# Performance work log

Hardware: AMD Instinct MI355X
Metric: run time of the kernel (lower is better)

The kernel has to match this reference:

```python
import jax, jax.numpy as jnp
import numpy as np

B, N, D = 16, 512, 256
HEADS = 8
HIDEF = 1024
BLOCK, WINDOW = 32, 64
LEVELS = 5
PYOUT = 128
NCLS, NANCH = 5, 9
NEG = -1e9


def _sinusoidal_pos(n, d):
    # PositionEmbeddingStatic: deterministic sinusoidal table [n, d]
    pos = np.arange(n)[:, None].astype(np.float64)
    i = np.arange(d)[None, :]
    angle = pos / np.power(10000.0, (2 * (i // 2)) / d)
    pe = np.where(i % 2 == 0, np.sin(angle), np.cos(angle))
    return jnp.asarray(pe, jnp.float32)


def _layernorm(x, g, b, eps=1e-5):
    m = x.mean(-1, keepdims=True)
    v = x.var(-1, keepdims=True)
    return (x - m) * jax.lax.rsqrt(v + eps) * g + b


def _bn(x_bcn, g, b, eps=1e-5):
    # BatchNorm1d in training mode: per-channel batch stats over (B, N)
    m = x_bcn.mean((0, 2), keepdims=True)
    v = x_bcn.var((0, 2), keepdims=True)
    return (x_bcn - m) * jax.lax.rsqrt(v + eps) * g[None, :, None] + b[None, :, None]


def _sparse_attention(x, Wqkv, bqkv, Wo, bo):
    # Windowed block-sparse attention: queries in block i attend to key blocks
    # [i-w, i+w] with w = window_size // block_size. Never materializes SxS.
    Bx, Nx, Dx = x.shape
    H, dh = HEADS, Dx // HEADS
    nb, bs = Nx // BLOCK, BLOCK
    w = WINDOW // BLOCK
    qkv = x @ Wqkv + bqkv
    q, k, v = jnp.split(qkv, 3, axis=-1)

    def to_blocks(t):  # [B,N,D] -> [B,H,nb,bs,dh]
        return t.reshape(Bx, nb, bs, H, dh).transpose(0, 3, 1, 2, 4)

    q, k, v = to_blocks(q), to_blocks(k), to_blocks(v)
    offs = list(range(-w, w + 1))
    # roll by -o puts key block (i+o) at query-block position i
    k_band = jnp.concatenate([jnp.roll(k, -o, axis=2) for o in offs], axis=3)
    v_band = jnp.concatenate([jnp.roll(v, -o, axis=2) for o in offs], axis=3)
    blk = jnp.arange(nb)
    valid = jnp.concatenate(
        [jnp.repeat(((blk + o >= 0) & (blk + o < nb))[:, None], bs, axis=1) for o in offs],
        axis=1)  # [nb, (2w+1)*bs]
    scale = 1.0 / jnp.sqrt(jnp.asarray(dh, x.dtype))
    scores = jnp.einsum('bhnqd,bhnkd->bhnqk', q, k_band) * scale
    scores = jnp.where(valid[None, None, :, None, :], scores, NEG)
    p = jax.nn.softmax(scores, axis=-1)
    o = jnp.einsum('bhnqk,bhnkd->bhnqd', p, v_band)
    o = o.transpose(0, 2, 3, 1, 4).reshape(Bx, Nx, Dx)
    return o @ Wo + bo


def setup_inputs():
    key = jax.random.key(0)
    ks = iter(jax.random.split(key, 48))
    g = lambda shape, s=0.02: jax.random.normal(next(ks), shape, jnp.float32) * s
    z = lambda *shape: jnp.zeros(shape, jnp.float32)
    o = lambda *shape: jnp.ones(shape, jnp.float32)
    return {
        'x': jax.random.normal(next(ks), (B, N, D), jnp.float32),
        'patch_W': g((D, D)), 'patch_b': z(D),
        'ln_g': o(D), 'ln_b': z(D),
        'ff_W1': g((D, HIDEF)), 'ff_b1': z(HIDEF),
        'ff_W2': g((HIDEF, D)), 'ff_b2': z(D),
        'Wqkv': g((D, 3 * D)), 'bqkv': z(3 * D),
        'Wo': g((D, D)), 'bo': z(D),
        'bn1_g': o(D), 'bn1_b': z(D),
        'bn2_g': o(D), 'bn2_b': z(D),
        'pyr_W': g((LEVELS, D, PYOUT)), 'pyr_b': z(LEVELS, PYOUT),
        'fcl_W': g((LEVELS * PYOUT * N, 128), 0.005), 'fcl_b': z(128),
        'addbn_g': o(128), 'addbn_b': z(128),
        'cls_W1': g((128, 256)), 'cls_b1': z(256),
        'cls_W2': g((256, NCLS * NANCH)), 'cls_b2': z(NCLS * NANCH),
        'box_W1': g((128, 128)), 'box_b1': z(128),
        'box_W2': g((128, 4 * NANCH)), 'box_b2': z(4 * NANCH),
    }


def reference(x, patch_W, patch_b, ln_g, ln_b, ff_W1, ff_b1, ff_W2, ff_b2,
              Wqkv, bqkv, Wo, bo, bn1_g, bn1_b, bn2_g, bn2_b,
              pyr_W, pyr_b, fcl_W, fcl_b, addbn_g, addbn_b,
              cls_W1, cls_b1, cls_W2, cls_b2, box_W1, box_b1, box_W2, box_b2):
    pos = _sinusoidal_pos(N, D)

    def ff(h):
        return jax.nn.gelu(h @ ff_W1 + ff_b1) @ ff_W2 + ff_b2

    def mnt(h):
        h = _layernorm(h @ patch_W + patch_b, ln_g, ln_b)  # patch embed + norm
        h = h + pos[None]
        idt = h
        h = ff(h)
        h = _sparse_attention(h, Wqkv, bqkv, Wo, bo)
        h = h + idt
        h = _bn(h.transpose(0, 2, 1), bn1_g, bn1_b).transpose(0, 2, 1)
        idt = h
        h = ff(h) + idt
        h = _bn(h.transpose(0, 2, 1), bn2_g, bn2_b).transpose(0, 2, 1)
        return h

    outs = []
    for _ in range(5):
        x = mnt(x)
        outs.append(x.transpose(0, 2, 1))  # [B, D, N]

    # pyramid: per-level 1x1 conv D -> 128
    feats = [jnp.einsum('bdn,dc->bcn', outs[i], pyr_W[i]) + pyr_b[i][None, :, None]
             for i in range(LEVELS)]
    flat = jnp.concatenate([f.reshape(f.shape[0], -1) for f in feats], axis=1)
    add = (flat @ fcl_W + fcl_b)[:, :, None]          # [B,128,1]
    add = _bn(add, addbn_g, addbn_b).transpose(0, 2, 1)  # [B,1,128]
    cls = jax.nn.relu(add @ cls_W1 + cls_b1) @ cls_W2 + cls_b2
    cls = jax.nn.softmax(cls, axis=-1).reshape(-1, NANCH, NCLS)  # eval mode softmax
    box = (jax.nn.relu(add @ box_W1 + box_b1) @ box_W2 + box_b2).reshape(-1, NANCH, 4)
    return jnp.concatenate([cls, box], axis=-1)  # [B, NANCH, NCLS+4]
```

## Files before the change

### kernel.cpp

```cpp
#include <hip/hip_runtime.h>
#include <hip/hip_bf16.h>
#include <math.h>

#define B_ 16
#define N_ 512
#define D_ 256
#define HEADS_ 8
#define DH_ 32
#define HIDEF_ 1024
#define NBLK_ 16
#define BS_ 32
#define LEVELS_ 5
#define PYOUT_ 128
#define ROWS_ (B_ * N_)
#define FCL_K 327680
#define FCL_KB 256
#define FCL_CHUNKS 1280

typedef __attribute__((ext_vector_type(8))) short short8;
typedef __attribute__((ext_vector_type(4))) short short4v;
typedef __attribute__((ext_vector_type(4))) unsigned short ushort4v;
typedef __attribute__((ext_vector_type(4))) float f32x4;

__device__ __forceinline__ float bf2f(short u) {
    return __uint_as_float(((unsigned int)(unsigned short)u) << 16);
}
__device__ __forceinline__ unsigned short f2bf(float x) {
    __hip_bfloat16 h = __float2bfloat16(x);
    return *reinterpret_cast<unsigned short*>(&h);
}

__device__ __forceinline__ float gelu_f(float x) {
    float x3 = x * x * x;
    return 0.5f * x * (1.f + tanhf(0.7978845608028654f * (x + 0.044715f * x3)));
}

__global__ __launch_bounds__(256) void prep_kernel(
    const float* __restrict__ patch_W, const float* __restrict__ Wqkv,
    const float* __restrict__ Wo, const float* __restrict__ ff_W1,
    const float* __restrict__ ff_W2, const float* __restrict__ pyr_W,
    const float* __restrict__ x_in,
    __hip_bfloat16* __restrict__ patchWt, __hip_bfloat16* __restrict__ qkvWt,
    __hip_bfloat16* __restrict__ WoWt, __hip_bfloat16* __restrict__ W1t,
    __hip_bfloat16* __restrict__ W2t, __hip_bfloat16* __restrict__ pyrWt,
    float* __restrict__ pos, __hip_bfloat16* __restrict__ Xb) {
    __shared__ float tt[32][33];
    int bid = blockIdx.x, t = threadIdx.x;
    if (bid >= 1504) {
        int base = (bid - 1504) * 2048 + t * 8;
        float4 a = *(const float4*)&x_in[base];
        float4 b = *(const float4*)&x_in[base + 4];
        ushort4v u0 = {f2bf(a.x), f2bf(a.y), f2bf(a.z), f2bf(a.w)};
        ushort4v u1 = {f2bf(b.x), f2bf(b.y), f2bf(b.z), f2bf(b.w)};
        *(ushort4v*)((short*)Xb + base) = u0;
        *(ushort4v*)((short*)Xb + base + 4) = u1;
        return;
    }
    if (bid >= 992) {
        int idx = (bid - 992) * 256 + t;
        int n = idx >> 8, i = idx & 255;
        double angle = (double)n / pow(10000.0, (double)(2 * (i >> 1)) / 256.0);
        pos[idx] = (float)((i & 1) ? cos(angle) : sin(angle));
        return;
    }
    const float* W; __hip_bfloat16* Wt; int K, N, bx, by;
    if (bid < 64)       { W = patch_W; Wt = patchWt; K = 256; N = 256; bx = bid % 8; by = bid / 8; }
    else if (bid < 256) { int l = bid - 64;  W = Wqkv;  Wt = qkvWt; K = 256; N = 768;  bx = l % 24; by = l / 24; }
    else if (bid < 320) { int l = bid - 256; W = Wo;    Wt = WoWt;  K = 256; N = 256;  bx = l % 8;  by = l / 8; }
    else if (bid < 576) { int l = bid - 320; W = ff_W1; Wt = W1t;   K = 256; N = 1024; bx = l % 32; by = l / 32; }
    else if (bid < 832) { int l = bid - 576; W = ff_W2; Wt = W2t;   K = 1024; N = 256; bx = l % 8;  by = l / 8; }
    else                { int l = bid - 832; int z = l / 32; int r = l % 32;
                          W = pyr_W + (size_t)z * 256 * 128; Wt = pyrWt + (size_t)z * 256 * 128;
                          K = 256; N = 128; bx = r % 4; by = r / 4; }
    int bx32 = bx * 32, by32 = by * 32;
    int tx = t & 31, ty = t >> 5;
#pragma unroll
    for (int i = 0; i < 32; i += 8)
        tt[ty + i][tx] = W[(size_t)(by32 + ty + i) * N + bx32 + tx];
    __syncthreads();
#pragma unroll
    for (int i = 0; i < 32; i += 8)
        Wt[(size_t)(bx32 + ty + i) * K + by32 + tx] = __float2bfloat16(tt[tx][ty + i]);
}

template <int ACT, bool OUTF, bool OUTB, bool STATS, int BM, int BN>
__global__ __launch_bounds__(256) void bgemm_kernel(
    const __hip_bfloat16* __restrict__ A, const __hip_bfloat16* __restrict__ Wt,
    const float* __restrict__ bias, const float* __restrict__ resid,
    float* __restrict__ C, __hip_bfloat16* __restrict__ Cb, int M, int Nn, int K,
    float* __restrict__ bnp) {
    __shared__ __hip_bfloat16 Alds[2][BM * 64];
    __shared__ __hip_bfloat16 Blds[2][BN * 64];
    constexpr int WM_ = (BM == 128 && BN == 64) ? 4 : 2;
    constexpr int WN_ = 4 / WM_;
    constexpr int WH = BM / WM_;
    constexpr int WC = BN / WN_;
    constexpr int MW = WH / 16;
    constexpr int NW = WC / 16;
    constexpr int AR = BM / 32;
    constexpr int BR = BN / 32;
    int tid = threadIdx.x;
    int wid = tid >> 6, lane = tid & 63;
    int flat = blockIdx.y * gridDim.x + blockIdx.x;
    int q8 = (gridDim.x * gridDim.y) >> 3;
    int wg = (flat & 7) * q8 + (flat >> 3);
    int bx = wg % gridDim.x, by = wg / gridDim.x;
    int row0 = by * BM, col0 = bx * BN;
    int wr = wid / WN_, wc = wid % WN_;
    int r16 = lane & 15, kq = lane >> 4;

    f32x4 acc[MW][NW];
#pragma unroll
    for (int m = 0; m < MW; m++)
#pragma unroll
        for (int n = 0; n < NW; n++) acc[m][n] = (f32x4){0.f, 0.f, 0.f, 0.f};

    auto stage = [&](int b, int k0) {
#pragma unroll
        for (int i = 0; i < AR; i++) {
            int slot = i * 256 + tid;
            int row = slot >> 3, qp = slot & 7;
            int q = qp ^ ((row >> 1) & 7);
            const __hip_bfloat16* ga = A + (size_t)(row0 + row) * K + k0 + q * 8;
            __builtin_amdgcn_global_load_lds(
                (const __attribute__((address_space(1))) void*)ga,
                (__attribute__((address_space(3))) void*)((char*)&Alds[b][0] + i * 4096 + wid * 1024),
                16, 0, 0);
        }
#pragma unroll
        for (int i = 0; i < BR; i++) {
            int slot = i * 256 + tid;
            int row = slot >> 3, qp = slot & 7;
            int q = qp ^ ((row >> 1) & 7);
            const __hip_bfloat16* gb = Wt + (size_t)(col0 + row) * K + k0 + q * 8;
            __builtin_amdgcn_global_load_lds(
                (const __attribute__((address_space(1))) void*)gb,
                (__attribute__((address_space(3))) void*)((char*)&Blds[b][0] + i * 4096 + wid * 1024),
                16, 0, 0);
        }
    };

    stage(0, 0);
    __syncthreads();
    int cur = 0;
    for (int k0 = 0; k0 < K; k0 += 64) {
        if (k0 + 64 < K) stage(cur ^ 1, k0 + 64);
#pragma unroll
        for (int h = 0; h < 2; h++) {
            short8 af[MW], bf4[NW];
#pragma unroll
            for (int m = 0; m < MW; m++) {
                int row = wr * WH + m * 16 + r16;
                int phys = (h * 4 + kq) ^ ((row >> 1) & 7);
                af[m] = *reinterpret_cast<const short8*>(
                    reinterpret_cast<const char*>(&Alds[cur][0]) + row * 128 + phys * 16);
            }
#pragma unroll
            for (int n = 0; n < NW; n++) {
                int row = wc * WC + n * 16 + r16;
                int phys = (h * 4 + kq) ^ ((row >> 1) & 7);
                bf4[n] = *reinterpret_cast<const short8*>(
                    reinterpret_cast<const char*>(&Blds[cur][0]) + row * 128 + phys * 16);
            }
#pragma unroll
            for (int m = 0; m < MW; m++)
#pragma unroll
                for (int n = 0; n < NW; n++)
                    acc[m][n] = __builtin_amdgcn_mfma_f32_16x16x32_bf16(af[m], bf4[n], acc[m][n], 0, 0, 0);
        }
        __syncthreads();
        cur ^= 1;
    }

    int rg = lane >> 4;
    float s1a[NW], s2a[NW];
#pragma unroll
    for (int n = 0; n < NW; n++) { s1a[n] = 0.f; s2a[n] = 0.f; }
#pragma unroll
    for (int n = 0; n < NW; n++) {
        int cc = col0 + wc * WC + n * 16 + r16;
        float bv = bias[cc];
#pragma unroll
        for (int m = 0; m < MW; m++) {
            int rb = row0 + wr * WH + m * 16 + rg * 4;
#pragma unroll
            for (int j = 0; j < 4; j++) {
                int r = rb + j;
                float v = acc[m][n][j] + bv;
                if (resid) v += resid[(size_t)r * Nn + cc];
                if (ACT == 1) v = gelu_f(v);
                if (OUTF) C[(size_t)r * Nn + cc] = v;
                if (OUTB) Cb[(size_t)r * Nn + cc] = __float2bfloat16(v);
                if (STATS) { s1a[n] += v; s2a[n] += v * v; }
            }
        }
    }
    if (STATS) {
        float* sc = (float*)&Alds[0][0];
        int part = wid * 4 + rg;
#pragma unroll
        for (int n = 0; n < NW; n++) {
            int c = wc * WC + n * 16 + r16;
            sc[c * 16 + part] = s1a[n];
            sc[BN * 16 + c * 16 + part] = s2a[n];
        }
        __syncthreads();
        if (tid < BN) {
            float a = 0.f, b2 = 0.f;
#pragma unroll
            for (int p = 0; p < 16; p++) {
                a += sc[tid * 16 + p];
                b2 += sc[BN * 16 + tid * 16 + p];
            }
            bnp[by * 256 + col0 + tid] = a;
            bnp[32768 + by * 256 + col0 + tid] = b2;
        }
    }
}

__global__ __launch_bounds__(256) void patchln_kernel(
    const __hip_bfloat16* __restrict__ A, const __hip_bfloat16* __restrict__ Wt,
    const float* __restrict__ bias, const float* __restrict__ lng,
    const float* __restrict__ lnb, const float* __restrict__ pos,
    float* __restrict__ H, __hip_bfloat16* __restrict__ Hb) {
    __shared__ char __attribute__((aligned(16))) smem[73728];
    float (*Cls)[260] = (float(*)[260])smem;
    int tid = threadIdx.x;
    int wid = tid >> 6, lane = tid & 63;
    int row0 = blockIdx.x * 32;
    int r16 = lane & 15, kq = lane >> 4, g = lane >> 4;

    f32x4 acc[2][4];
#pragma unroll
    for (int m = 0; m < 2; m++)
#pragma unroll
        for (int n = 0; n < 4; n++) acc[m][n] = (f32x4){0.f, 0.f, 0.f, 0.f};

    auto stage = [&](int b, int k0) {
        {
            int row = tid >> 3, qp = tid & 7;
            int q = qp ^ ((row >> 1) & 7);
            const __hip_bfloat16* ga = A + (size_t)(row0 + row) * 256 + k0 + q * 8;
            __builtin_amdgcn_global_load_lds(
                (const __attribute__((address_space(1))) void*)ga,
                (__attribute__((address_space(3))) void*)(smem + b * 4096 + wid * 1024),
                16, 0, 0);
        }
#pragma unroll
        for (int i = 0; i < 8; i++) {
            int slot = i * 256 + tid;
            int row = slot >> 3, qp = slot & 7;
            int q = qp ^ ((row >> 1) & 7);
            const __hip_bfloat16* gb = Wt + (size_t)row * 256 + k0 + q * 8;
            __builtin_amdgcn_global_load_lds(
                (const __attribute__((address_space(1))) void*)gb,
                (__attribute__((address_space(3))) void*)(smem + 8192 + b * 32768 + i * 4096 + wid * 1024),
                16, 0, 0);
        }
    };

    stage(0, 0);
    __syncthreads();
    int cur = 0;
    for (int k0 = 0; k0 < 256; k0 += 64) {
        if (k0 + 64 < 256) stage(cur ^ 1, k0 + 64);
        const char* Ab = smem + cur * 4096;
        const char* Bb = smem + 8192 + cur * 32768;
#pragma unroll
        for (int h = 0; h < 2; h++) {
            short8 af[2], bf4[4];
#pragma unroll
            for (int m = 0; m < 2; m++) {
                int row = m * 16 + r16;
                int phys = (h * 4 + kq) ^ ((row >> 1) & 7);
                af[m] = *reinterpret_cast<const short8*>(Ab + row * 128 + phys * 16);
            }
#pragma unroll
            for (int n = 0; n < 4; n++) {
                int row = wid * 64 + n * 16 + r16;
                int phys = (h * 4 + kq) ^ ((row >> 1) & 7);
                bf4[n] = *reinterpret_cast<const short8*>(Bb + row * 128 + phys * 16);
            }
#pragma unroll
            for (int m = 0; m < 2; m++)
#pragma unroll
                for (int n = 0; n < 4; n++)
                    acc[m][n] = __builtin_amdgcn_mfma_f32_16x16x32_bf16(af[m], bf4[n], acc[m][n], 0, 0, 0);
        }
        __syncthreads();
        cur ^= 1;
    }
#pragma unroll
    for (int n = 0; n < 4; n++) {
        int col = wid * 64 + n * 16 + r16;
        float bv = bias[col];
#pragma unroll
        for (int m = 0; m < 2; m++)
#pragma unroll
            for (int j = 0; j < 4; j++)
                Cls[m * 16 + g * 4 + j][col] = acc[m][n][j] + bv;
    }
    __syncthreads();
    float4 g4 = ((const float4*)lng)[lane];
    float4 b4 = ((const float4*)lnb)[lane];
#pragma unroll
    for (int rr = 0; rr < 8; rr++) {
        int r = wid * 8 + rr;
        float4 v = *(const float4*)&Cls[r][lane * 4];
        float s = v.x + v.y + v.z + v.w;
#pragma unroll
        for (int mk = 32; mk; mk >>= 1) s += __shfl_xor(s, mk);
        float mean = s * (1.f / 256.f);
        float dx = v.x - mean, dy = v.y - mean, dz = v.z - mean, dw = v.w - mean;
        float q = dx * dx + dy * dy + dz * dz + dw * dw;
#pragma unroll
        for (int mk = 32; mk; mk >>= 1) q += __shfl_xor(q, mk);
        float rstd = rsqrtf(q * (1.f / 256.f) + 1e-5f);
        int grow = row0 + r;
        float4 p4 = ((const float4*)pos)[(size_t)(grow & (N_ - 1)) * 64 + lane];
        float o0 = dx * rstd * g4.x + b4.x + p4.x;
        float o1 = dy * rstd * g4.y + b4.y + p4.y;
        float o2 = dz * rstd * g4.z + b4.z + p4.z;
        float o3 = dw * rstd * g4.w + b4.w + p4.w;
        ((float4*)(H + (size_t)grow * D_))[lane] = (float4){o0, o1, o2, o3};
        ushort4v u = {f2bf(o0), f2bf(o1), f2bf(o2), f2bf(o3)};
        *((ushort4v*)(Hb + (size_t)grow * D_) + lane) = u;
    }
}

template <bool DO_PATCH>
__global__ __launch_bounds__(256) void bnpatch_kernel(
    const float* __restrict__ T, const float* __restrict__ bnp,
    const float* __restrict__ bng, const float* __restrict__ bnb,
    const __hip_bfloat16* __restrict__ patchWt, const float* __restrict__ patch_b,
    const float* __restrict__ lng, const float* __restrict__ lnb,
    const float* __restrict__ pos,
    const __hip_bfloat16* __restrict__ pyrWt_l, const float* __restrict__ pyr_b_l,
    int level, float* __restrict__ FLAT,
    float* __restrict__ H, __hip_bfloat16* __restrict__ Hb) {
    __shared__ char __attribute__((aligned(16))) smem[68096];
    float* sm = (float*)(smem + 66048);
    float* sv = sm + 256;
    int tid = threadIdx.x;
    int wid = tid >> 6, lane = tid & 63;
    int row0 = blockIdx.x * 32;
    int r16 = lane & 15, kq = lane >> 4, g = lane >> 4;
    int wr = wid >> 1, wc = wid & 1;

    {
        float s = 0.f, s2 = 0.f;
#pragma unroll 4
        for (int yy = 0; yy < 128; yy++) {
            s += bnp[yy * 256 + tid];
            s2 += bnp[32768 + yy * 256 + tid];
        }
        float m = s * (1.f / 8192.f);
        sm[tid] = m;
        sv[tid] = rsqrtf(s2 * (1.f / 8192.f) - m * m + 1e-5f);
    }
    __syncthreads();
    {
        float4 m4 = ((const float4*)sm)[lane];
        float4 r4 = ((const float4*)sv)[lane];
        float4 g4 = ((const float4*)bng)[lane];
        float4 b4 = ((const float4*)bnb)[lane];
#pragma unroll
        for (int rr = 0; rr < 8; rr++) {
            int r = wid * 8 + rr;
            float4 x4 = ((const float4*)(T + (size_t)(row0 + r) * D_))[lane];
            float o0 = (x4.x - m4.x) * r4.x * g4.x + b4.x;
            float o1 = (x4.y - m4.y) * r4.y * g4.y + b4.y;
            float o2 = (x4.z - m4.z) * r4.z * g4.z + b4.z;
            float o3 = (x4.w - m4.w) * r4.w * g4.w + b4.w;
            ushort4v u = {f2bf(o0), f2bf(o1), f2bf(o2), f2bf(o3)};
            int c = lane >> 1;
            int phys = c ^ (r & 7);
            *(ushort4v*)(smem + r * 512 + phys * 16 + (lane & 1) * 8) = u;
        }
    }
    __syncthreads();

    if (DO_PATCH) {
        f32x4 acc[8];
#pragma unroll
        for (int n = 0; n < 8; n++) acc[n] = (f32x4){0.f, 0.f, 0.f, 0.f};
        for (int k0 = 0; k0 < 256; k0 += 64) {
#pragma unroll
            for (int i = 0; i < 8; i++) {
                int slot = i * 256 + tid;
                int row = slot >> 3, qp = slot & 7;
                int q = qp ^ ((row >> 1) & 7);
                const __hip_bfloat16* gb = patchWt + (size_t)row * 256 + k0 + q * 8;
                __builtin_amdgcn_global_load_lds(
                    (const __attribute__((address_space(1))) void*)gb,
                    (__attribute__((address_space(3))) void*)(smem + 16384 + i * 4096 + wid * 1024),
                    16, 0, 0);
            }
            __syncthreads();
#pragma unroll
            for (int h = 0; h < 2; h++) {
                int arow = wr * 16 + r16;
                int ac = (k0 >> 3) + h * 4 + kq;
                int aphys = ac ^ (arow & 7);
                short8 af = *(const short8*)(smem + arow * 512 + aphys * 16);
                short8 bf4[8];
#pragma unroll
                for (int n = 0; n < 8; n++) {
                    int brow = wc * 128 + n * 16 + r16;
                    int bphys = (h * 4 + kq) ^ ((brow >> 1) & 7);
                    bf4[n] = *(const short8*)(smem + 16384 + brow * 128 + bphys * 16);
                }
#pragma unroll
                for (int n = 0; n < 8; n++)
                    acc[n] = __builtin_amdgcn_mfma_f32_16x16x32_bf16(af, bf4[n], acc[n], 0, 0, 0);
            }
            __syncthreads();
        }
        float (*Cls)[260] = (float(*)[260])(smem + 16384);
#pragma unroll
        for (int n = 0; n < 8; n++) {
            int col = wc * 128 + n * 16 + r16;
            float bv = patch_b[col];
#pragma unroll
            for (int j = 0; j < 4; j++)
                Cls[wr * 16 + g * 4 + j][col] = acc[n][j] + bv;
        }
        __syncthreads();
        float4 g4 = ((const float4*)lng)[lane];
        float4 b4 = ((const float4*)lnb)[lane];
#pragma unroll
        for (int rr = 0; rr < 8; rr++) {
            int r = wid * 8 + rr;
            float4 v = *(const float4*)&Cls[r][lane * 4];
            float s = v.x + v.y + v.z + v.w;
#pragma unroll
            for (int mk = 32; mk; mk >>= 1) s += __shfl_xor(s, mk);
            float mean = s * (1.f / 256.f);
            float dx = v.x - mean, dy = v.y - mean, dz = v.z - mean, dw = v.w - mean;
            float q = dx * dx + dy * dy + dz * dz + dw * dw;
#pragma unroll
            for (int mk = 32; mk; mk >>= 1) q += __shfl_xor(q, mk);
            float rstd = rsqrtf(q * (1.f / 256.f) + 1e-5f);
            int grow = row0 + r;
            float4 p4 = ((const float4*)pos)[(size_t)(grow & (N_ - 1)) * 64 + lane];
            float o0 = dx * rstd * g4.x + b4.x + p4.x;
            float o1 = dy * rstd * g4.y + b4.y + p4.y;
            float o2 = dz * rstd * g4.z + b4.z + p4.z;
            float o3 = dw * rstd * g4.w + b4.w + p4.w;
            ((float4*)(H + (size_t)grow * D_))[lane] = (float4){o0, o1, o2, o3};
            ushort4v u = {f2bf(o0), f2bf(o1), f2bf(o2), f2bf(o3)};
            *((ushort4v*)(Hb + (size_t)grow * D_) + lane) = u;
        }
    }

    f32x4 pacc[4];
#pragma unroll
    for (int n = 0; n < 4; n++) pacc[n] = (f32x4){0.f, 0.f, 0.f, 0.f};
    for (int k0 = 0; k0 < 256; k0 += 64) {
#pragma unroll
        for (int i = 0; i < 4; i++) {
            int slot = i * 256 + tid;
            int row = slot >> 3, qp = slot & 7;
            int q = qp ^ ((row >> 1) & 7);
            const __hip_bfloat16* gb = pyrWt_l + (size_t)row * 256 + k0 + q * 8;
            __builtin_amdgcn_global_load_lds(
                (const __attribute__((address_space(1))) void*)gb,
                (__attribute__((address_space(3))) void*)(smem + 49664 + i * 4096 + wid * 1024),
                16, 0, 0);
        }
        __syncthreads();
#pragma unroll
        for (int h = 0; h < 2; h++) {
            int arow = wr * 16 + r16;
            int ac = (k0 >> 3) + h * 4 + kq;
            int aphys = ac ^ (arow & 7);
            short8 af = *(const short8*)(smem + arow * 512 + aphys * 16);
            short8 bf4[4];
#pragma unroll
            for (int n = 0; n < 4; n++) {
                int brow = wc * 64 + n * 16 + r16;
                int bphys = (h * 4 + kq) ^ ((brow >> 1) & 7);
                bf4[n] = *(const short8*)(smem + 49664 + brow * 128 + bphys * 16);
            }
#pragma unroll
            for (int n = 0; n < 4; n++)
                pacc[n] = __builtin_amdgcn_mfma_f32_16x16x32_bf16(af, bf4[n], pacc[n], 0, 0, 0);
        }
        __syncthreads();
    }
    float (*olds)[33] = (float(*)[33])(smem + 16384);
#pragma unroll
    for (int n = 0; n < 4; n++) {
        int ch = wc * 64 + n * 16 + r16;
        float bv = pyr_b_l[ch];
#pragma unroll
        for (int j = 0; j < 4; j++)
            olds[ch][wr * 16 + g * 4 + j] = pacc[n][j] + bv;
    }
    __syncthreads();
    {
        int ch = tid >> 1, half = tid & 1;
        int bb = row0 >> 9, nn0 = (row0 & 511) + half * 16;
        float* dst = FLAT + (size_t)bb * 327680 + (size_t)(level * 128 + ch) * 512 + nn0;
        const float* src = &olds[ch][half * 16];
#pragma unroll
        for (int q = 0; q < 4; q++)
            *(float4*)(dst + q * 4) = *(const float4*)(src + q * 4);
    }
}

__global__ __launch_bounds__(256) void bn_applyfin_kernel(
    const float* __restrict__ x, const float* __restrict__ bnp, int prows,
    const float* __restrict__ g, const float* __restrict__ b,
    float* __restrict__ y, __hip_bfloat16* __restrict__ yb) {
    int tid = threadIdx.x;
    __shared__ float sm[256], sv[256];
    {
        float s = 0.f, s2 = 0.f;
#pragma unroll 4
        for (int yy = 0; yy < prows; yy++) {
            s += bnp[yy * 256 + tid];
            s2 += bnp[32768 + yy * 256 + tid];
        }
        float m = s * (1.f / 8192.f);
        sm[tid] = m;
        sv[tid] = rsqrtf(s2 * (1.f / 8192.f) - m * m + 1e-5f);
    }
    __syncthreads();
    int lane = tid & 63, w = tid >> 6;
    int row0 = blockIdx.x * 32;
    float4 m4 = *(const float4*)&sm[lane * 4];
    float4 r4 = *(const float4*)&sv[lane * 4];
    float4 g4 = ((const float4*)g)[lane];
    float4 b4 = ((const float4*)b)[lane];
#pragma unroll
    for (int rr = 0; rr < 8; rr++) {
        int row = row0 + w * 8 + rr;
        float4 x4 = ((const float4*)(x + (size_t)row * D_))[lane];
        float o0 = (x4.x - m4.x) * r4.x * g4.x + b4.x;
        float o1 = (x4.y - m4.y) * r4.y * g4.y + b4.y;
        float o2 = (x4.z - m4.z) * r4.z * g4.z + b4.z;
        float o3 = (x4.w - m4.w) * r4.w * g4.w + b4.w;
        if (y) ((float4*)(y + (size_t)row * D_))[lane] = (float4){o0, o1, o2, o3};
        if (yb) {
            ushort4v u = {f2bf(o0), f2bf(o1), f2bf(o2), f2bf(o3)};
            *((ushort4v*)(yb + (size_t)row * D_) + lane) = u;
        }
    }
}

__global__ __launch_bounds__(256) void attn_kernel(
    const __hip_bfloat16* __restrict__ qkv, __hip_bfloat16* __restrict__ outb) {
    int bx = blockIdx.x, h = blockIdx.y, b = blockIdx.z;
    int tid = threadIdx.x;
    int wid = tid >> 6, lane = tid & 63;
    __shared__ __hip_bfloat16 Klds[256 * 32];
    __shared__ __hip_bfloat16 Vt[32 * 264];
    const short* q16 = (const short*)qkv;

#pragma unroll
    for (int r = 0; r < 4; r++) {
        int slot = r * 256 + tid;
        int row = slot >> 2, qp = slot & 3;
        int ql = qp ^ ((row >> 1) & 3);
        int jb = bx * 4 - 2 + (row >> 5);
        jb = jb < 0 ? 0 : (jb > 15 ? 15 : jb);
        const short* ga = q16 + ((size_t)(b * N_ + jb * 32 + (row & 31))) * 768 + 256 + h * 32 + ql * 8;
        __builtin_amdgcn_global_load_lds(
            (const __attribute__((address_space(1))) void*)ga,
            (__attribute__((address_space(3))) void*)((char*)Klds + r * 4096 + wid * 1024),
            16, 0, 0);
    }
    {
        int row = tid;
        int jb = bx * 4 - 2 + (row >> 5);
        jb = jb < 0 ? 0 : (jb > 15 ? 15 : jb);
        const short* gv = q16 + ((size_t)(b * N_ + jb * 32 + (row & 31))) * 768 + 512 + h * 32;
        short8 v0 = *(const short8*)(gv);
        short8 v1 = *(const short8*)(gv + 8);
        short8 v2 = *(const short8*)(gv + 16);
        short8 v3 = *(const short8*)(gv + 24);
        short* vt = (short*)Vt;
#pragma unroll
        for (int e = 0; e < 8; e++) {
            vt[(e) * 264 + row] = v0[e];
            vt[(8 + e) * 264 + row] = v1[e];
            vt[(16 + e) * 264 + row] = v2[e];
            vt[(24 + e) * 264 + row] = v3[e];
        }
    }
    __syncthreads();

    int i = bx * 4 + wid;
    int c = lane & 15, g = lane >> 4;
    const float scale = 0.17677669529663687f;

#pragma unroll
    for (int qt = 0; qt < 2; qt++) {
        const short* qa = q16 + ((size_t)(b * N_ + i * 32 + qt * 16 + c)) * 768 + h * 32 + g * 8;
        short8 bq = *(const short8*)qa;
        f32x4 st[10];
#pragma unroll
        for (int t = 0; t < 10; t++) {
            int jb = i - 2 + (t >> 1);
            if (jb >= 0 && jb < NBLK_) {
                int row = wid * 32 + t * 16 + c;
                int phys = g ^ ((row >> 1) & 3);
                short8 ak = *(const short8*)((const char*)Klds + row * 64 + phys * 16);
                st[t] = __builtin_amdgcn_mfma_f32_16x16x32_bf16(
                    ak, bq, (f32x4){0.f, 0.f, 0.f, 0.f}, 0, 0, 0);
            }
        }
        float mx = -1e30f;
#pragma unroll
        for (int t = 0; t < 10; t++) {
            int jb = i - 2 + (t >> 1);
            if (jb >= 0 && jb < NBLK_) {
#pragma unroll
                for (int j = 0; j < 4; j++) {
                    st[t][j] *= scale;
                    mx = fmaxf(mx, st[t][j]);
                }
            }
        }
        mx = fmaxf(mx, __shfl_xor(mx, 16));
        mx = fmaxf(mx, __shfl_xor(mx, 32));
        float sum = 0.f;
#pragma unroll
        for (int t = 0; t < 10; t++) {
            int jb = i - 2 + (t >> 1);
            if (jb >= 0 && jb < NBLK_) {
#pragma unroll
                for (int j = 0; j < 4; j++) {
                    float e = __expf(st[t][j] - mx);
                    st[t][j] = e;
                    sum += e;
                }
            }
        }
        sum += __shfl_xor(sum, 16);
        sum += __shfl_xor(sum, 32);
        float inv = 1.f / sum;
        f32x4 o0 = (f32x4){0.f, 0.f, 0.f, 0.f};
        f32x4 o1 = (f32x4){0.f, 0.f, 0.f, 0.f};
        const short* vt = (const short*)Vt;
#pragma unroll
        for (int t = 0; t < 10; t++) {
            int jb = i - 2 + (t >> 1);
            if (jb >= 0 && jb < NBLK_) {
                short8 pa = (short8)0;
#pragma unroll
                for (int j = 0; j < 4; j++) pa[j] = (short)f2bf(st[t][j] * inv);
                int kb = wid * 32 + t * 16 + g * 4;
                short4v vb0 = *(const short4v*)(vt + (0 * 16 + c) * 264 + kb);
                short4v vb1 = *(const short4v*)(vt + (1 * 16 + c) * 264 + kb);
                short8 b0 = (short8)0, b1 = (short8)0;
#pragma unroll
                for (int e = 0; e < 4; e++) { b0[e] = vb0[e]; b1[e] = vb1[e]; }
                o0 = __builtin_amdgcn_mfma_f32_16x16x32_bf16(pa, b0, o0, 0, 0, 0);
                o1 = __builtin_amdgcn_mfma_f32_16x16x32_bf16(pa, b1, o1, 0, 0, 0);
            }
        }
#pragma unroll
        for (int j = 0; j < 4; j++) {
            size_t rbase = ((size_t)(b * N_ + i * 32 + qt * 16 + g * 4 + j)) * D_ + h * DH_;
            outb[rbase + c] = __float2bfloat16(o0[j]);
            outb[rbase + 16 + c] = __float2bfloat16(o1[j]);
        }
    }
}

__global__ __launch_bounds__(256) void fcl_partial_kernel(
    const float* __restrict__ flat, const float* __restrict__ W,
    float* __restrict__ partial) {
    int chunk = blockIdx.x;
    int t = threadIdx.x;
    int k0 = chunk * FCL_KB;
    __shared__ float fl[FCL_KB][20];
#pragma unroll
    for (int b = 0; b < 16; b++)
        fl[t][b] = flat[(size_t)b * FCL_K + k0 + t];
    __syncthreads();
    int j = t & 127, bg = t >> 7;
    f32x4 a0 = (f32x4){0.f, 0.f, 0.f, 0.f};
    f32x4 a1 = (f32x4){0.f, 0.f, 0.f, 0.f};
#pragma unroll 8
    for (int k = 0; k < FCL_KB; k++) {
        float w = W[(size_t)(k0 + k) * 128 + j];
        f32x4 f0 = *(const f32x4*)&fl[k][bg * 8];
        f32x4 f1 = *(const f32x4*)&fl[k][bg * 8 + 4];
        a0 += f0 * w;
        a1 += f1 * w;
    }
#pragma unroll
    for (int bi = 0; bi < 4; bi++) {
        partial[((size_t)chunk * 16 + bg * 8 + bi) * 128 + j] = a0[bi];
        partial[((size_t)chunk * 16 + bg * 8 + 4 + bi) * 128 + j] = a1[bi];
    }
}

__global__ __launch_bounds__(256) void fcl_reduce_kernel(
    const float* __restrict__ partial, const float* __restrict__ fcl_b,
    float* __restrict__ add) {
    int c0 = blockIdx.x * 32;
    int t = threadIdx.x;
    int ry = t >> 5, cx = t & 31;
    float s = 0.f;
    for (int r = ry; r < FCL_CHUNKS; r += 8)
        s += partial[(size_t)r * 2048 + c0 + cx];
    __shared__ float red[8][32];
    red[ry][cx] = s; __syncthreads();
    if (ry == 0) {
        float tot = 0.f;
#pragma unroll
        for (int q = 0; q < 8; q++) tot += red[q][cx];
        int col = c0 + cx;
        add[col] = tot + fcl_b[col & 127];
    }
}

__global__ __launch_bounds__(256) void head_kernel(
    const float* __restrict__ add, const float* __restrict__ abg, const float* __restrict__ abb,
    const float* __restrict__ cls_W1, const float* __restrict__ cls_b1,
    const float* __restrict__ cls_W2, const float* __restrict__ cls_b2,
    const float* __restrict__ box_W1, const float* __restrict__ box_b1,
    const float* __restrict__ box_W2, const float* __restrict__ box_b2,
    float* __restrict__ out) {
    __shared__ float a2[16][128];
    __shared__ float cm[16][256];
    __shared__ float cls[16][45];
    __shared__ float bmid[16][128];
    __shared__ float smden[16];
    int t = threadIdx.x;
    if (t < 128) {
        float m = 0.f;
#pragma unroll
        for (int b = 0; b < 16; b++) m += add[b * 128 + t];
        m *= (1.f / 16.f);
        float v = 0.f;
#pragma unroll
        for (int b = 0; b < 16; b++) { float d = add[b * 128 + t] - m; v += d * d; }
        v *= (1.f / 16.f);
        float sc = rsqrtf(v + 1e-5f) * abg[t];
#pragma unroll
        for (int b = 0; b < 16; b++) a2[b][t] = (add[b * 128 + t] - m) * sc + abb[t];
    }
    __syncthreads();
    for (int idx = t; idx < 4096; idx += 256) {
        int m = idx >> 8, c = idx & 255;
        float a = cls_b1[c];
        for (int k = 0; k < 128; k++) a += a2[m][k] * cls_W1[k * 256 + c];
        cm[m][c] = fmaxf(a, 0.f);
    }
    for (int idx = t; idx < 2048; idx += 256) {
        int m = idx >> 7, c = idx & 127;
        float a = box_b1[c];
        for (int k = 0; k < 128; k++) a += a2[m][k] * box_W1[k * 128 + c];
        bmid[m][c] = fmaxf(a, 0.f);
    }
    __syncthreads();
    for (int idx = t; idx < 720; idx += 256) {
        int m = idx / 45, c = idx % 45;
        float a = cls_b2[c];
        for (int k = 0; k < 256; k++) a += cm[m][k] * cls_W2[k * 45 + c];
        cls[m][c] = a;
    }
    __syncthreads();
    if (t < 16) {
        float mx = -1e30f;
        for (int c = 0; c < 45; c++) mx = fmaxf(mx, cls[t][c]);
        float s = 0.f;
        for (int c = 0; c < 45; c++) { float e = expf(cls[t][c] - mx); cls[t][c] = e; s += e; }
        smden[t] = s;
    }
    for (int idx = t; idx < 576; idx += 256) {
        int m = idx / 36, c = idx % 36;
        float a = box_b2[c];
        for (int k = 0; k < 128; k++) a += bmid[m][k] * box_W2[k * 36 + c];
        out[m * 81 + (c >> 2) * 9 + 5 + (c & 3)] = a;
    }
    __syncthreads();
    for (int idx = t; idx < 720; idx += 256) {
        int m = idx / 45, c = idx % 45;
        out[m * 81 + (c / 5) * 9 + (c % 5)] = cls[m][c] / smden[m];
    }
}

extern "C" void kernel_launch(void* const* d_in, const int* in_sizes, int n_in,
                              void* d_out, int out_size, void* d_ws, size_t ws_size,
                              hipStream_t stream) {
    const float* x_in    = (const float*)d_in[0];
    const float* patch_W = (const float*)d_in[1];
    const float* patch_b = (const float*)d_in[2];
    const float* ln_g    = (const float*)d_in[3];
    const float* ln_b    = (const float*)d_in[4];
    const float* ff_W1   = (const float*)d_in[5];
    const float* ff_b1   = (const float*)d_in[6];
    const float* ff_W2   = (const float*)d_in[7];
    const float* ff_b2   = (const float*)d_in[8];
    const float* Wqkv    = (const float*)d_in[9];
    const float* bqkv    = (const float*)d_in[10];
    const float* Wo      = (const float*)d_in[11];
    const float* bo      = (const float*)d_in[12];
    const float* bn1_g   = (const float*)d_in[13];
    const float* bn1_b   = (const float*)d_in[14];
    const float* bn2_g   = (const float*)d_in[15];
    const float* bn2_b   = (const float*)d_in[16];
    const float* pyr_W   = (const float*)d_in[17];
    const float* pyr_b   = (const float*)d_in[18];
    const float* fcl_W   = (const float*)d_in[19];
    const float* fcl_b   = (const float*)d_in[20];
    const float* addbn_g = (const float*)d_in[21];
    const float* addbn_b = (const float*)d_in[22];
    const float* cls_W1  = (const float*)d_in[23];
    const float* cls_b1  = (const float*)d_in[24];
    const float* cls_W2  = (const float*)d_in[25];
    const float* cls_b2  = (const float*)d_in[26];
    const float* box_W1  = (const float*)d_in[27];
    const float* box_b1  = (const float*)d_in[28];
    const float* box_W2  = (const float*)d_in[29];
    const float* box_b2  = (const float*)d_in[30];
    float* out = (float*)d_out;

    float* ws = (float*)d_ws;
    size_t off = 0;
    float* POS   = ws + off; off += 131072;
    float* H     = ws + off; off += 2097152;
    float* T     = ws + off; off += 2097152;
    float* UNION = ws + off; off += 4194304;
    float* FLAT  = ws + off; off += 5242880;
    float* PART  = ws + off; off += (size_t)FCL_CHUNKS * 2048;
    float* BNP   = ws + off; off += 2 * 32768;
    float* ADD   = ws + off; off += 2048;
    __hip_bfloat16* Hb   = (__hip_bfloat16*)(ws + off); off += 1048576;
    __hip_bfloat16* Tb   = (__hip_bfloat16*)(ws + off); off += 1048576;
    __hip_bfloat16* Xb   = (__hip_bfloat16*)(ws + off); off += 1048576;
    __hip_bfloat16* ATb  = (__hip_bfloat16*)(ws + off); off += 1048576;
    __hip_bfloat16* patchWt = (__hip_bfloat16*)(ws + off); off += 32768;
    __hip_bfloat16* qkvWt   = (__hip_bfloat16*)(ws + off); off += 98304;
    __hip_bfloat16* WoWt    = (__hip_bfloat16*)(ws + off); off += 32768;
    __hip_bfloat16* W1t     = (__hip_bfloat16*)(ws + off); off += 131072;
    __hip_bfloat16* W2t     = (__hip_bfloat16*)(ws + off); off += 131072;
    __hip_bfloat16* pyrWt   = (__hip_bfloat16*)(ws + off); off += 81920;
    __hip_bfloat16* MIDb = (__hip_bfloat16*)UNION;
    __hip_bfloat16* QKVb = (__hip_bfloat16*)UNION;

    prep_kernel<<<2528, 256, 0, stream>>>(
        patch_W, Wqkv, Wo, ff_W1, ff_W2, pyr_W, x_in,
        patchWt, qkvWt, WoWt, W1t, W2t, pyrWt, POS, Xb);

    patchln_kernel<<<256, 256, 0, stream>>>(Xb, patchWt, patch_b, ln_g, ln_b, POS, H, Hb);

    for (int it = 0; it < 5; it++) {
        bgemm_kernel<1, false, true, false, 128, 128><<<dim3(8, 64), 256, 0, stream>>>(
            Hb, W1t, ff_b1, nullptr, nullptr, MIDb, ROWS_, HIDEF_, D_, nullptr);
        bgemm_kernel<0, false, true, false, 64, 64><<<dim3(4, 128), 256, 0, stream>>>(
            MIDb, W2t, ff_b2, nullptr, nullptr, Tb, ROWS_, D_, HIDEF_, nullptr);
        bgemm_kernel<0, false, true, false, 128, 64><<<dim3(12, 64), 256, 0, stream>>>(
            Tb, qkvWt, bqkv, nullptr, nullptr, QKVb, ROWS_, 768, D_, nullptr);
        attn_kernel<<<dim3(4, HEADS_, B_), 256, 0, stream>>>(QKVb, ATb);
        bgemm_kernel<0, true, false, true, 64, 64><<<dim3(4, 128), 256, 0, stream>>>(
            ATb, WoWt, bo, H, T, nullptr, ROWS_, D_, D_, BNP);
        bn_applyfin_kernel<<<256, 256, 0, stream>>>(T, BNP, 128, bn1_g, bn1_b, H, Hb);
        bgemm_kernel<1, false, true, false, 128, 128><<<dim3(8, 64), 256, 0, stream>>>(
            Hb, W1t, ff_b1, nullptr, nullptr, MIDb, ROWS_, HIDEF_, D_, nullptr);
        bgemm_kernel<0, true, false, true, 64, 64><<<dim3(4, 128), 256, 0, stream>>>(
            MIDb, W2t, ff_b2, H, T, nullptr, ROWS_, D_, HIDEF_, BNP);
        if (it < 4) {
            bnpatch_kernel<true><<<256, 256, 0, stream>>>(
                T, BNP, bn2_g, bn2_b, patchWt, patch_b, ln_g, ln_b, POS,
                pyrWt + (size_t)it * D_ * PYOUT_, pyr_b + it * PYOUT_, it, FLAT, H, Hb);
        } else {
            bnpatch_kernel<false><<<256, 256, 0, stream>>>(
                T, BNP, bn2_g, bn2_b, patchWt, patch_b, ln_g, ln_b, POS,
                pyrWt + (size_t)it * D_ * PYOUT_, pyr_b + it * PYOUT_, it, FLAT, H, Hb);
        }
    }

    fcl_partial_kernel<<<FCL_CHUNKS, 256, 0, stream>>>(FLAT, fcl_W, PART);
    fcl_reduce_kernel<<<64, 256, 0, stream>>>(PART, fcl_b, ADD);
    head_kernel<<<1, 256, 0, stream>>>(ADD, addbn_g, addbn_b,
        cls_W1, cls_b1, cls_W2, cls_b2, box_W1, box_b1, box_W2, box_b2, out);
    (void)in_sizes; (void)n_in; (void)out_size; (void)ws_size;
}
```

Before: 873.1 us.

## Fuse BatchNorm apply into first FFN GEMM prologue

Replaces the separate BN1 apply kernel and the following FFN up-projection GEMM with one kernel. Each 64x128 tile recomputes the BN statistics from the partial sums, normalizes its 64 rows of T into swizzled LDS as bf16, and runs an MFMA GEMM against W1 staged with async global-to-LDS loads. This removes a launch and the round trip of the bf16 activation through global memory. In exchange every one of the 1024 workgroups repeats the 128-row stats reduction and the T row reads (8x redundant across column tiles).

```diff
diff --git a/kernel.cpp b/kernel.cpp
--- a/kernel.cpp
+++ b/kernel.cpp
@@ -218,6 +218,123 @@
     }
 }
 
+__global__ __launch_bounds__(256) void bnff1_kernel(
+    const float* __restrict__ T, const float* __restrict__ bnp,
+    const float* __restrict__ bng, const float* __restrict__ bnb,
+    const __hip_bfloat16* __restrict__ W1t, const float* __restrict__ ff_b1,
+    float* __restrict__ H, __hip_bfloat16* __restrict__ MIDb) {
+    __shared__ char __attribute__((aligned(16))) smem[67584];
+    float* sm = (float*)(smem + 65536);
+    float* sv = sm + 256;
+    int tid = threadIdx.x;
+    int wid = tid >> 6, lane = tid & 63;
+    int flat = blockIdx.y * gridDim.x + blockIdx.x;
+    int q8 = (gridDim.x * gridDim.y) >> 3;
+    int wg = (flat & 7) * q8 + (flat >> 3);
+    int bx = wg & 7, by = wg >> 3;
+    int row0 = by * 64, col0 = bx * 128;
+    int r16 = lane & 15, kq = lane >> 4, rg = lane >> 4;
+
+    {
+        float s = 0.f, s2 = 0.f;
+#pragma unroll 4
+        for (int yy = 0; yy < 128; yy++) {
+            s += bnp[yy * 256 + tid];
+            s2 += bnp[32768 + yy * 256 + tid];
+        }
+        float m = s * (1.f / 8192.f);
+        sm[tid] = m;
+        sv[tid] = rsqrtf(s2 * (1.f / 8192.f) - m * m + 1e-5f);
+    }
+    __syncthreads();
+    {
+        float4 m4 = ((const float4*)sm)[lane];
+        float4 r4 = ((const float4*)sv)[lane];
+        float4 g4 = ((const float4*)bng)[lane];
+        float4 b4 = ((const float4*)bnb)[lane];
+#pragma unroll
+        for (int rr = 0; rr < 16; rr++) {
+            int r = wid * 16 + rr;
+            int grow = row0 + r;
+            float4 x4 = ((const float4*)(T + (size_t)grow * D_))[lane];
+            float o0 = (x4.x - m4.x) * r4.x * g4.x + b4.x;
+            float o1 = (x4.y - m4.y) * r4.y * g4.y + b4.y;
+            float o2 = (x4.z - m4.z) * r4.z * g4.z + b4.z;
+            float o3 = (x4.w - m4.w) * r4.w * g4.w + b4.w;
+            ushort4v u = {f2bf(o0), f2bf(o1), f2bf(o2), f2bf(o3)};
+            int c = lane >> 1;
+            int phys = c ^ (r & 7);
+            *(ushort4v*)(smem + r * 512 + phys * 16 + (lane & 1) * 8) = u;
+            if (bx == 0)
+                ((float4*)(H + (size_t)grow * D_))[lane] = (float4){o0, o1, o2, o3};
+        }
+    }
+    auto stageB = [&](int b, int k0) {
+#pragma unroll
+        for (int i = 0; i < 4; i++) {
+            int slot = i * 256 + tid;
+            int row = slot >> 3, qp = slot & 7;
+            int q = qp ^ ((row >> 1) & 7);
+            const __hip_bfloat16* gb = W1t + (size_t)(col0 + row) * 256 + k0 + q * 8;
+            __builtin_amdgcn_global_load_lds(
+                (const __attribute__((address_space(1))) void*)gb,
+                (__attribute__((address_space(3))) void*)(smem + 32768 + b * 16384 + i * 4096 + wid * 1024),
+                16, 0, 0);
+        }
+    };
+    f32x4 acc[4][2];
+#pragma unroll
+    for (int m = 0; m < 4; m++)
+#pragma unroll
+        for (int n = 0; n < 2; n++) acc[m][n] = (f32x4){0.f, 0.f, 0.f, 0.f};
+    stageB(0, 0);
+    __syncthreads();
+    int cur = 0;
+    for (int k0 = 0; k0 < 256; k0 += 64) {
+        if (k0 + 64 < 256) stageB(cur ^ 1, k0 + 64);
+        const char* Bb = smem + 32768 + cur * 16384;
+#pragma unroll
+        for (int h = 0; h < 2; h++) {
+            int ac = (k0 >> 3) + h * 4 + kq;
+            short8 af[4];
+#pragma unroll
+            for (int m = 0; m < 4; m++) {
+                int arow = m * 16 + r16;
+                int aphys = ac ^ (arow & 7);
+                af[m] = *(const short8*)(smem + arow * 512 + aphys * 16);
+            }
+            short8 bf4[2];
+#pragma unroll
+            for (int n = 0; n < 2; n++) {
+                int brow = wid * 32 + n * 16 + r16;
+                int bphys = (h * 4 + kq) ^ ((brow >> 1) & 7);
+                bf4[n] = *(const short8*)(Bb + brow * 128 + bphys * 16);
+            }
+#pragma unroll
+            for (int m = 0; m < 4; m++)
+#pragma unroll
+                for (int n = 0; n < 2; n++)
+                    acc[m][n] = __builtin_amdgcn_mfma_f32_16x16x32_bf16(af[m], bf4[n], acc[m][n], 0, 0, 0);
+        }
+        __syncthreads();
+        cur ^= 1;
+    }
+#pragma unroll
+    for (int n = 0; n < 2; n++) {
+        int cc = col0 + wid * 32 + n * 16 + r16;
+        float bv = ff_b1[cc];
+#pragma unroll
+        for (int m = 0; m < 4; m++) {
+            int rb = row0 + m * 16 + rg * 4;
+#pragma unroll
+            for (int j = 0; j < 4; j++) {
+                float v = gelu_f(acc[m][n][j] + bv);
+                MIDb[(size_t)(rb + j) * HIDEF_ + cc] = __float2bfloat16(v);
+            }
+        }
+    }
+}
+
 __global__ __launch_bounds__(256) void patchln_kernel(
     const __hip_bfloat16* __restrict__ A, const __hip_bfloat16* __restrict__ Wt,
     const float* __restrict__ bias, const float* __restrict__ lng,
@@ -506,46 +623,6 @@
 #pragma unroll
         for (int q = 0; q < 4; q++)
             *(float4*)(dst + q * 4) = *(const float4*)(src + q * 4);
-    }
-}
-
-__global__ __launch_bounds__(256) void bn_applyfin_kernel(
-    const float* __restrict__ x, const float* __restrict__ bnp, int prows,
-    const float* __restrict__ g, const float* __restrict__ b,
-    float* __restrict__ y, __hip_bfloat16* __restrict__ yb) {
-    int tid = threadIdx.x;
-    __shared__ float sm[256], sv[256];
-    {
-        float s = 0.f, s2 = 0.f;
-#pragma unroll 4
-        for (int yy = 0; yy < prows; yy++) {
-            s += bnp[yy * 256 + tid];
-            s2 += bnp[32768 + yy * 256 + tid];
-        }
-        float m = s * (1.f / 8192.f);
-        sm[tid] = m;
-        sv[tid] = rsqrtf(s2 * (1.f / 8192.f) - m * m + 1e-5f);
-    }
-    __syncthreads();
-    int lane = tid & 63, w = tid >> 6;
-    int row0 = blockIdx.x * 32;
-    float4 m4 = *(const float4*)&sm[lane * 4];
-    float4 r4 = *(const float4*)&sv[lane * 4];
-    float4 g4 = ((const float4*)g)[lane];
-    float4 b4 = ((const float4*)b)[lane];
-#pragma unroll
-    for (int rr = 0; rr < 8; rr++) {
-        int row = row0 + w * 8 + rr;
-        float4 x4 = ((const float4*)(x + (size_t)row * D_))[lane];
-        float o0 = (x4.x - m4.x) * r4.x * g4.x + b4.x;
-        float o1 = (x4.y - m4.y) * r4.y * g4.y + b4.y;
-        float o2 = (x4.z - m4.z) * r4.z * g4.z + b4.z;
-        float o3 = (x4.w - m4.w) * r4.w * g4.w + b4.w;
-        if (y) ((float4*)(y + (size_t)row * D_))[lane] = (float4){o0, o1, o2, o3};
-        if (yb) {
-            ushort4v u = {f2bf(o0), f2bf(o1), f2bf(o2), f2bf(o3)};
-            *((ushort4v*)(yb + (size_t)row * D_) + lane) = u;
-        }
     }
 }
 
@@ -861,9 +938,8 @@
         attn_kernel<<<dim3(4, HEADS_, B_), 256, 0, stream>>>(QKVb, ATb);
         bgemm_kernel<0, true, false, true, 64, 64><<<dim3(4, 128), 256, 0, stream>>>(
             ATb, WoWt, bo, H, T, nullptr, ROWS_, D_, D_, BNP);
-        bn_applyfin_kernel<<<256, 256, 0, stream>>>(T, BNP, 128, bn1_g, bn1_b, H, Hb);
-        bgemm_kernel<1, false, true, false, 128, 128><<<dim3(8, 64), 256, 0, stream>>>(
-            Hb, W1t, ff_b1, nullptr, nullptr, MIDb, ROWS_, HIDEF_, D_, nullptr);
+        bnff1_kernel<<<dim3(8, 128), 256, 0, stream>>>(
+            T, BNP, bn1_g, bn1_b, W1t, ff_b1, H, MIDb);
         bgemm_kernel<0, true, false, true, 64, 64><<<dim3(4, 128), 256, 0, stream>>>(
             MIDb, W2t, ff_b2, H, T, nullptr, ROWS_, D_, HIDEF_, BNP);
         if (it < 4) {
```

After: 898.5 us. +2.9%, slower.
